# Kernel optimization log

Measured on AMD Instinct MI355X. Metric: run time of the kernel, lower is better.

## Reference

```python
import jax, jax.numpy as jnp
import numpy as np

N_ATOMS = 100_000   # atom_node.size(0)
N_EDGES = 3_200_000  # avg degree 32


def setup_inputs() -> dict:
    key = jax.random.key(0)
    k1, k2, k3, k4, k5 = jax.random.split(key, 5)
    disp = jax.random.normal(k1, (N_EDGES, 3), dtype=jnp.float32)
    a = jax.random.normal(k2, (N_EDGES,), dtype=jnp.float32)
    b = jax.random.normal(k3, (N_EDGES,), dtype=jnp.float32)
    edge_index = jax.random.randint(k4, (2, N_EDGES), 0, N_ATOMS, dtype=jnp.int64)
    atom_node = jax.random.randint(k5, (N_ATOMS,), 0, 100, dtype=jnp.int64)
    return {"disp": disp, "a": a, "b": b, "edge_index": edge_index, "atom_node": atom_node}


def _energy(disp, a, b):
    # surrogate differentiable per-edge energy: E = sum_e a_e*r2_e + b_e*exp(-r2_e)
    r2 = jnp.sum(disp * disp, axis=-1)  # [E]
    return jnp.sum(a * r2 + b * jnp.exp(-r2))


def reference(disp, a, b, edge_index, atom_node):
    n = atom_node.shape[0]
    # force = -dE/d(disp), create_graph analog: jax grads are differentiable
    force_edge = -jax.grad(_energy, argnums=0)(disp, a, b)  # [E,3]
    # dual scatter-add over the two endpoint index rows, then subtract
    f_src = jax.ops.segment_sum(force_edge, edge_index[0], num_segments=n)  # [N,3]
    f_dst = jax.ops.segment_sum(force_edge, edge_index[1], num_segments=n)  # [N,3]
    return f_src - f_dst
```

## Files before the change

kernel.cpp:

```cpp
#include <hip/hip_runtime.h>
#include <hip/hip_bf16.h>
#include <hip/hip_fp16.h>
#include <math.h>
#include <stdint.h>

constexpr int TPB         = 256;
constexpr int U           = 4;
constexpr int ROUND_EDGES = TPB * U;
constexpr int ROUND_REC   = ROUND_EDGES * 2;
constexpr int EPB         = 2048;
constexpr int NPB_SHIFT   = 10;
constexpr int NODES_PER_B = 1 << NPB_SHIFT;
constexpr int NB_MAX      = 128;
constexpr int CAPREC      = 80000;
constexpr int SPLIT       = 16;
constexpr int OCAP        = 262144;

__device__ __forceinline__ uint64_t pack_rec(int local, float fx, float fy, float fz) {
    uint64_t hx = __half_as_ushort(__float2half(fx));
    uint64_t hy = __half_as_ushort(__float2half(fy));
    uint64_t hz = __half_as_ushort(__float2half(fz));
    return (uint64_t)(unsigned)local | (hx << 16) | (hy << 32) | (hz << 48);
}

__global__ void __launch_bounds__(TPB)
p1_partition(const float* __restrict__ disp,
             const float* __restrict__ a,
             const float* __restrict__ b,
             const int* __restrict__ src,
             const int* __restrict__ dst,
             uint64_t* __restrict__ grecords,
             int* __restrict__ gcur,
             uint4* __restrict__ ovf,
             int* __restrict__ ovf_cnt,
             int E, int NB) {
    __shared__ int      s_cnt[NB_MAX];
    __shared__ int      s_off[NB_MAX];
    __shared__ int      s_gd[NB_MAX];
    __shared__ uint64_t s_rec[ROUND_REC];
    __shared__ uint8_t  s_bin[ROUND_REC];

    const int t = threadIdx.x;
    const int base = blockIdx.x * EPB;
    const int bend = min(base + EPB, E);

    for (int rb = base; rb < bend; rb += ROUND_EDGES) {
        const int rend = min(rb + ROUND_EDGES, bend);
        if (t < NB_MAX) s_cnt[t] = 0;
        __syncthreads();

        const int e0 = rb + t * U;
        float dxv[U], dyv[U], dzv[U], av[U], bv[U];
        int sv[U], dv[U];
        bool valid[U];
        if (e0 + U <= rend) {
            const float4* p = (const float4*)(disp + (size_t)3 * e0);
            float4 q0 = p[0], q1 = p[1], q2 = p[2];
            dxv[0] = q0.x; dyv[0] = q0.y; dzv[0] = q0.z;
            dxv[1] = q0.w; dyv[1] = q1.x; dzv[1] = q1.y;
            dxv[2] = q1.z; dyv[2] = q1.w; dzv[2] = q2.x;
            dxv[3] = q2.y; dyv[3] = q2.z; dzv[3] = q2.w;
            float4 qa = *(const float4*)(a + e0);
            av[0] = qa.x; av[1] = qa.y; av[2] = qa.z; av[3] = qa.w;
            float4 qb = *(const float4*)(b + e0);
            bv[0] = qb.x; bv[1] = qb.y; bv[2] = qb.z; bv[3] = qb.w;
            int4 qs = *(const int4*)(src + e0);
            sv[0] = qs.x; sv[1] = qs.y; sv[2] = qs.z; sv[3] = qs.w;
            int4 qd = *(const int4*)(dst + e0);
            dv[0] = qd.x; dv[1] = qd.y; dv[2] = qd.z; dv[3] = qd.w;
#pragma unroll
            for (int u = 0; u < U; ++u) valid[u] = true;
        } else {
#pragma unroll
            for (int u = 0; u < U; ++u) {
                int e = e0 + u;
                valid[u] = (e < rend);
                if (valid[u]) {
                    dxv[u] = disp[3 * e + 0];
                    dyv[u] = disp[3 * e + 1];
                    dzv[u] = disp[3 * e + 2];
                    av[u] = a[e]; bv[u] = b[e];
                    sv[u] = src[e]; dv[u] = dst[e];
                }
            }
        }

        uint64_t rec[2 * U];
        int rbin[2 * U], rrank[2 * U];
#pragma unroll
        for (int u = 0; u < U; ++u) {
            if (valid[u]) {
                float dx = dxv[u], dy = dyv[u], dz = dzv[u];
                float r2 = dx * dx + dy * dy + dz * dz;
                float coef = -2.0f * (av[u] - bv[u] * __expf(-r2));
                float fx = coef * dx, fy = coef * dy, fz = coef * dz;
                int nds[2] = { sv[u], dv[u] };
#pragma unroll
                for (int j = 0; j < 2; ++j) {
                    int k = 2 * u + j;
                    float s = j ? -1.0f : 1.0f;
                    int node = nds[j];
                    rec[k] = pack_rec(node & (NODES_PER_B - 1), s * fx, s * fy, s * fz);
                    rbin[k] = node >> NPB_SHIFT;
                    rrank[k] = atomicAdd(&s_cnt[rbin[k]], 1);
                }
            } else {
                rbin[2 * u] = -1; rbin[2 * u + 1] = -1;
            }
        }
        __syncthreads();

        if (t < 64) {
            int v0 = s_cnt[t];
            int v1 = s_cnt[64 + t];
#pragma unroll
            for (int d = 1; d < 64; d <<= 1) {
                int u0 = __shfl_up(v0, d, 64);
                int u1 = __shfl_up(v1, d, 64);
                if (t >= d) { v0 += u0; v1 += u1; }
            }
            int total0 = __shfl(v0, 63, 64);
            s_off[t] = v0;
            s_off[64 + t] = v1 + total0;
        }
        __syncthreads();

        if (t < NB) {
            int c = s_cnt[t];
            if (c > 0)
                s_gd[t] = atomicAdd(&gcur[t], c) - (s_off[t] - c);
        }
#pragma unroll
        for (int k = 0; k < 2 * U; ++k) {
            if (rbin[k] >= 0) {
                int pos = s_off[rbin[k]] - s_cnt[rbin[k]] + rrank[k];
                s_rec[pos] = rec[k];
                s_bin[pos] = (uint8_t)rbin[k];
            }
        }
        __syncthreads();

        const int total = s_off[NB_MAX - 1];
        for (int i = t; i < total; i += TPB) {
            uint64_t q = s_rec[i];
            int bin = (int)s_bin[i];
            int pos = s_gd[bin] + i;
            if ((unsigned)pos < (unsigned)CAPREC) {
                grecords[(size_t)bin * CAPREC + pos] = q;
            } else {
                int o = atomicAdd(ovf_cnt, 1);
                if (o < OCAP) {
                    uint4 v;
                    v.x = (unsigned)((bin << NPB_SHIFT) | (int)(q & (NODES_PER_B - 1)));
                    v.y = __float_as_uint(__half2float(__ushort_as_half((unsigned short)(q >> 16))));
                    v.z = __float_as_uint(__half2float(__ushort_as_half((unsigned short)(q >> 32))));
                    v.w = __float_as_uint(__half2float(__ushort_as_half((unsigned short)(q >> 48))));
                    ovf[o] = v;
                }
            }
        }
        __syncthreads();
    }
}

__device__ __forceinline__ uint64_t enc_xyz(float vx, float vy, float vz) {
    vx = fminf(fmaxf(vx, -63.0f), 63.0f);
    vy = fminf(fmaxf(vy, -63.0f), 63.0f);
    vz = fminf(fmaxf(vz, -63.0f), 63.0f);
    unsigned ex = (unsigned)((int)rintf(vx * 64.0f) + 4096);
    unsigned ey = (unsigned)((int)rintf(vy * 64.0f) + 4096);
    unsigned ez = (unsigned)((int)rintf(vz * 64.0f) + 4096);
    return (1ull << 54) | ((uint64_t)ez << 36) | ((uint64_t)ey << 18) | (uint64_t)ex;
}

__global__ void __launch_bounds__(TPB)
p2_reduce(const uint64_t* __restrict__ grecords,
          const int* __restrict__ gcur,
          float* __restrict__ partials,
          int NB) {
    __shared__ unsigned long long accA[NODES_PER_B];
    const int t = threadIdx.x;
    const int bucket = blockIdx.x >> 4;
    const int part   = blockIdx.x & (SPLIT - 1);

    for (int i = t; i < NODES_PER_B; i += TPB) accA[i] = 0ull;
    __syncthreads();

    int n = gcur[bucket];
    if (n > CAPREC) n = CAPREC;
    int lo = (int)((long long)n * part / SPLIT);
    int hi = (int)((long long)n * (part + 1) / SPLIT);
    const uint64_t* rbase = grecords + (size_t)bucket * CAPREC;

    int i = lo + t;
    for (; i + 3 * TPB < hi; i += 4 * TPB) {
        uint64_t q0 = rbase[i];
        uint64_t q1 = rbase[i + TPB];
        uint64_t q2 = rbase[i + 2 * TPB];
        uint64_t q3 = rbase[i + 3 * TPB];
#pragma unroll
        for (int u = 0; u < 4; ++u) {
            uint64_t q = (u == 0) ? q0 : (u == 1) ? q1 : (u == 2) ? q2 : q3;
            int local = (int)(q & (NODES_PER_B - 1));
            float vx = __half2float(__ushort_as_half((unsigned short)(q >> 16)));
            float vy = __half2float(__ushort_as_half((unsigned short)(q >> 32)));
            float vz = __half2float(__ushort_as_half((unsigned short)(q >> 48)));
            atomicAdd(&accA[local], (unsigned long long)enc_xyz(vx, vy, vz));
        }
    }
    for (; i < hi; i += TPB) {
        uint64_t q = rbase[i];
        int local = (int)(q & (NODES_PER_B - 1));
        float vx = __half2float(__ushort_as_half((unsigned short)(q >> 16)));
        float vy = __half2float(__ushort_as_half((unsigned short)(q >> 32)));
        float vz = __half2float(__ushort_as_half((unsigned short)(q >> 48)));
        atomicAdd(&accA[local], (unsigned long long)enc_xyz(vx, vy, vz));
    }
    __syncthreads();

    float* pb = partials + (size_t)part * ((size_t)NB * NODES_PER_B * 3)
              + (size_t)bucket * NODES_PER_B * 3;
    for (int k = t; k < NODES_PER_B; k += TPB) {
        uint64_t A = accA[k];
        float cnt = (float)(unsigned)(A >> 54);
        float xf = (float)(int)(A & 0x3FFFFull);
        float yf = (float)(int)((A >> 18) & 0x3FFFFull);
        float zf = (float)(int)((A >> 36) & 0x3FFFFull);
        float bias = cnt * 4096.0f;
        pb[k * 3 + 0] = (xf - bias) * (1.0f / 64.0f);
        pb[k * 3 + 1] = (yf - bias) * (1.0f / 64.0f);
        pb[k * 3 + 2] = (zf - bias) * (1.0f / 64.0f);
    }
}

__global__ void __launch_bounds__(TPB)
p4_sum_partials(const float* __restrict__ partials, float* __restrict__ out,
                int out_size, size_t pstride) {
    int i = blockIdx.x * blockDim.x + threadIdx.x;
    if (i >= out_size) return;
    float s = 0.0f;
#pragma unroll
    for (int p = 0; p < SPLIT; ++p)
        s += partials[(size_t)p * pstride + i];
    out[i] = s;
}

__global__ void __launch_bounds__(TPB)
p3_overflow(const uint4* __restrict__ ovf, const int* __restrict__ ovf_cnt,
            float* __restrict__ out) {
    int n = *ovf_cnt;
    if (n > OCAP) n = OCAP;
    int stride = gridDim.x * blockDim.x;
    for (int i = blockIdx.x * blockDim.x + threadIdx.x; i < n; i += stride) {
        uint4 r = ovf[i];
        int node = (int)r.x;
        unsafeAtomicAdd(&out[node * 3 + 0], __uint_as_float(r.y));
        unsafeAtomicAdd(&out[node * 3 + 1], __uint_as_float(r.z));
        unsafeAtomicAdd(&out[node * 3 + 2], __uint_as_float(r.w));
    }
}

__global__ void __launch_bounds__(TPB)
edge_force_scatter_direct(const float* __restrict__ disp,
                          const float* __restrict__ a,
                          const float* __restrict__ b,
                          const int* __restrict__ src,
                          const int* __restrict__ dst,
                          float* __restrict__ out,
                          int E) {
    int e = blockIdx.x * blockDim.x + threadIdx.x;
    if (e >= E) return;
    float dx = disp[3 * e + 0], dy = disp[3 * e + 1], dz = disp[3 * e + 2];
    float r2 = dx * dx + dy * dy + dz * dz;
    float coef = -2.0f * (a[e] - b[e] * __expf(-r2));
    float fx = coef * dx, fy = coef * dy, fz = coef * dz;
    int s = 3 * src[e], d = 3 * dst[e];
    unsafeAtomicAdd(&out[s + 0], fx);
    unsafeAtomicAdd(&out[s + 1], fy);
    unsafeAtomicAdd(&out[s + 2], fz);
    unsafeAtomicAdd(&out[d + 0], -fx);
    unsafeAtomicAdd(&out[d + 1], -fy);
    unsafeAtomicAdd(&out[d + 2], -fz);
}

extern "C" void kernel_launch(void* const* d_in, const int* in_sizes, int n_in,
                              void* d_out, int out_size, void* d_ws, size_t ws_size,
                              hipStream_t stream) {
    const float* disp = (const float*)d_in[0];
    const float* a    = (const float*)d_in[1];
    const float* b    = (const float*)d_in[2];
    const int*   ei   = (const int*)d_in[3];

    int E = in_sizes[1];
    int N = in_sizes[4];
    float* out = (float*)d_out;

    int NB = (N + NODES_PER_B - 1) >> NPB_SHIFT;
    int NBLK = (E + EPB - 1) / EPB;
    size_t pstride = (size_t)NB * NODES_PER_B * 3;

    size_t rec_bytes = (size_t)NB * CAPREC * sizeof(uint64_t);
    size_t need = 1024
                + rec_bytes
                + (size_t)OCAP * sizeof(uint4)
                + (size_t)SPLIT * pstride * sizeof(float);

    if (NB <= NB_MAX && ws_size >= need) {
        char* wsb = (char*)d_ws;
        int* gcur          = (int*)wsb;
        int* ovf_cnt       = (int*)(wsb + NB_MAX * sizeof(int));
        uint64_t* grecords = (uint64_t*)(wsb + 1024);
        uint4* ovf         = (uint4*)(wsb + 1024 + rec_bytes);
        float* partials    = (float*)((char*)ovf + (size_t)OCAP * sizeof(uint4));

        (void)hipMemsetAsync(wsb, 0, 1024, stream);

        p1_partition<<<NBLK, TPB, 0, stream>>>(
            disp, a, b, ei, ei + E, grecords, gcur, ovf, ovf_cnt, E, NB);
        p2_reduce<<<NB * SPLIT, TPB, 0, stream>>>(
            grecords, gcur, partials, NB);
        int grid4 = (out_size + TPB - 1) / TPB;
        p4_sum_partials<<<grid4, TPB, 0, stream>>>(partials, out, out_size, pstride);
        p3_overflow<<<64, TPB, 0, stream>>>(ovf, ovf_cnt, out);
    } else {
        (void)hipMemsetAsync(d_out, 0, (size_t)out_size * sizeof(float), stream);
        int grid = (E + TPB - 1) / TPB;
        edge_force_scatter_direct<<<grid, TPB, 0, stream>>>(
            disp, a, b, ei, ei + E, out, E);
    }
}
```

Measured before the change: 185.4 us.

## Replace global per-bucket atomic cursors with fixed per-block bucket slots

The partition kernel no longer does atomicAdd on a shared per-bucket cursor. Each block now writes its records into a private fixed-capacity slot region (CAP=56) per bucket and records its count. The reduce kernel walks all slots per bucket and skips empty entries using the per-block counts, with SPLIT cut from 16 to 8. This removes global atomic contention and makes write offsets deterministic. The cost is padded storage, wasted reads of empty slots and per-record divide/count checks, and blocks whose count exceeds CAP spill to the slower overflow path.

```diff
diff --git a/kernel.cpp b/kernel.cpp
--- a/kernel.cpp
+++ b/kernel.cpp
@@ -12,8 +12,8 @@
 constexpr int NPB_SHIFT   = 10;
 constexpr int NODES_PER_B = 1 << NPB_SHIFT;
 constexpr int NB_MAX      = 128;
-constexpr int CAPREC      = 80000;
-constexpr int SPLIT       = 16;
+constexpr int CAP         = 56;
+constexpr int SPLIT       = 8;
 constexpr int OCAP        = 262144;
 
 __device__ __forceinline__ uint64_t pack_rec(int local, float fx, float fy, float fz) {
@@ -30,10 +30,10 @@
              const int* __restrict__ src,
              const int* __restrict__ dst,
              uint64_t* __restrict__ grecords,
-             int* __restrict__ gcur,
+             int* __restrict__ gcnt,
              uint4* __restrict__ ovf,
              int* __restrict__ ovf_cnt,
-             int E, int NB) {
+             int E, int NB, int NBLK) {
     __shared__ int      s_cnt[NB_MAX];
     __shared__ int      s_off[NB_MAX];
     __shared__ int      s_gd[NB_MAX];
@@ -41,8 +41,11 @@
     __shared__ uint8_t  s_bin[ROUND_REC];
 
     const int t = threadIdx.x;
-    const int base = blockIdx.x * EPB;
+    const int blk = blockIdx.x;
+    const int base = blk * EPB;
     const int bend = min(base + EPB, E);
+
+    int wcur = 0;
 
     for (int rb = base; rb < bend; rb += ROUND_EDGES) {
         const int rend = min(rb + ROUND_EDGES, bend);
@@ -127,8 +130,8 @@
 
         if (t < NB) {
             int c = s_cnt[t];
-            if (c > 0)
-                s_gd[t] = atomicAdd(&gcur[t], c) - (s_off[t] - c);
+            s_gd[t] = wcur - (s_off[t] - c);
+            wcur += c;
         }
 #pragma unroll
         for (int k = 0; k < 2 * U; ++k) {
@@ -145,8 +148,8 @@
             uint64_t q = s_rec[i];
             int bin = (int)s_bin[i];
             int pos = s_gd[bin] + i;
-            if ((unsigned)pos < (unsigned)CAPREC) {
-                grecords[(size_t)bin * CAPREC + pos] = q;
+            if ((unsigned)pos < (unsigned)CAP) {
+                grecords[((size_t)bin * NBLK + blk) * CAP + pos] = q;
             } else {
                 int o = atomicAdd(ovf_cnt, 1);
                 if (o < OCAP) {
@@ -161,6 +164,8 @@
         }
         __syncthreads();
     }
+
+    if (t < NB) gcnt[(size_t)t * NBLK + blk] = min(wcur, CAP);
 }
 
 __device__ __forceinline__ uint64_t enc_xyz(float vx, float vy, float vz) {
@@ -175,46 +180,57 @@
 
 __global__ void __launch_bounds__(TPB)
 p2_reduce(const uint64_t* __restrict__ grecords,
-          const int* __restrict__ gcur,
+          const int* __restrict__ gcnt,
           float* __restrict__ partials,
-          int NB) {
+          int NB, int NBLK) {
     __shared__ unsigned long long accA[NODES_PER_B];
     const int t = threadIdx.x;
-    const int bucket = blockIdx.x >> 4;
+    const int bucket = blockIdx.x >> 3;
     const int part   = blockIdx.x & (SPLIT - 1);
 
     for (int i = t; i < NODES_PER_B; i += TPB) accA[i] = 0ull;
     __syncthreads();
 
-    int n = gcur[bucket];
-    if (n > CAPREC) n = CAPREC;
-    int lo = (int)((long long)n * part / SPLIT);
-    int hi = (int)((long long)n * (part + 1) / SPLIT);
-    const uint64_t* rbase = grecords + (size_t)bucket * CAPREC;
+    const int totslots = NBLK * CAP;
+    int lo = (int)((long long)totslots * part / SPLIT);
+    int hi = (int)((long long)totslots * (part + 1) / SPLIT);
+    const uint64_t* rbase = grecords + (size_t)bucket * totslots;
+    const int*      cbase = gcnt     + (size_t)bucket * NBLK;
 
     int i = lo + t;
     for (; i + 3 * TPB < hi; i += 4 * TPB) {
-        uint64_t q0 = rbase[i];
-        uint64_t q1 = rbase[i + TPB];
-        uint64_t q2 = rbase[i + 2 * TPB];
-        uint64_t q3 = rbase[i + 3 * TPB];
+        bool v[4]; uint64_t q[4];
 #pragma unroll
         for (int u = 0; u < 4; ++u) {
-            uint64_t q = (u == 0) ? q0 : (u == 1) ? q1 : (u == 2) ? q2 : q3;
-            int local = (int)(q & (NODES_PER_B - 1));
-            float vx = __half2float(__ushort_as_half((unsigned short)(q >> 16)));
-            float vy = __half2float(__ushort_as_half((unsigned short)(q >> 32)));
-            float vz = __half2float(__ushort_as_half((unsigned short)(q >> 48)));
+            int j = i + u * TPB;
+            int nb = j / CAP;
+            int slot = j - nb * CAP;
+            v[u] = slot < cbase[nb];
+            q[u] = v[u] ? rbase[j] : 0ull;
+        }
+#pragma unroll
+        for (int u = 0; u < 4; ++u) {
+            if (v[u]) {
+                uint64_t q0 = q[u];
+                int local = (int)(q0 & (NODES_PER_B - 1));
+                float vx = __half2float(__ushort_as_half((unsigned short)(q0 >> 16)));
+                float vy = __half2float(__ushort_as_half((unsigned short)(q0 >> 32)));
+                float vz = __half2float(__ushort_as_half((unsigned short)(q0 >> 48)));
+                atomicAdd(&accA[local], (unsigned long long)enc_xyz(vx, vy, vz));
+            }
+        }
+    }
+    for (; i < hi; i += TPB) {
+        int nb = i / CAP;
+        int slot = i - nb * CAP;
+        if (slot < cbase[nb]) {
+            uint64_t q0 = rbase[i];
+            int local = (int)(q0 & (NODES_PER_B - 1));
+            float vx = __half2float(__ushort_as_half((unsigned short)(q0 >> 16)));
+            float vy = __half2float(__ushort_as_half((unsigned short)(q0 >> 32)));
+            float vz = __half2float(__ushort_as_half((unsigned short)(q0 >> 48)));
             atomicAdd(&accA[local], (unsigned long long)enc_xyz(vx, vy, vz));
         }
-    }
-    for (; i < hi; i += TPB) {
-        uint64_t q = rbase[i];
-        int local = (int)(q & (NODES_PER_B - 1));
-        float vx = __half2float(__ushort_as_half((unsigned short)(q >> 16)));
-        float vy = __half2float(__ushort_as_half((unsigned short)(q >> 32)));
-        float vz = __half2float(__ushort_as_half((unsigned short)(q >> 48)));
-        atomicAdd(&accA[local], (unsigned long long)enc_xyz(vx, vy, vz));
     }
     __syncthreads();
 
@@ -299,26 +315,28 @@
     int NBLK = (E + EPB - 1) / EPB;
     size_t pstride = (size_t)NB * NODES_PER_B * 3;
 
-    size_t rec_bytes = (size_t)NB * CAPREC * sizeof(uint64_t);
-    size_t need = 1024
+    size_t gcnt_bytes = (((size_t)NB * NBLK * sizeof(int)) + 255) & ~(size_t)255;
+    size_t rec_bytes  = (size_t)NB * NBLK * CAP * sizeof(uint64_t);
+    size_t need = 256
+                + gcnt_bytes
                 + rec_bytes
                 + (size_t)OCAP * sizeof(uint4)
                 + (size_t)SPLIT * pstride * sizeof(float);
 
     if (NB <= NB_MAX && ws_size >= need) {
         char* wsb = (char*)d_ws;
-        int* gcur          = (int*)wsb;
-        int* ovf_cnt       = (int*)(wsb + NB_MAX * sizeof(int));
-        uint64_t* grecords = (uint64_t*)(wsb + 1024);
-        uint4* ovf         = (uint4*)(wsb + 1024 + rec_bytes);
+        int* ovf_cnt       = (int*)wsb;
+        int* gcnt          = (int*)(wsb + 256);
+        uint64_t* grecords = (uint64_t*)(wsb + 256 + gcnt_bytes);
+        uint4* ovf         = (uint4*)(wsb + 256 + gcnt_bytes + rec_bytes);
         float* partials    = (float*)((char*)ovf + (size_t)OCAP * sizeof(uint4));
 
-        (void)hipMemsetAsync(wsb, 0, 1024, stream);
+        (void)hipMemsetAsync(wsb, 0, 256, stream);
 
         p1_partition<<<NBLK, TPB, 0, stream>>>(
-            disp, a, b, ei, ei + E, grecords, gcur, ovf, ovf_cnt, E, NB);
+            disp, a, b, ei, ei + E, grecords, gcnt, ovf, ovf_cnt, E, NB, NBLK);
         p2_reduce<<<NB * SPLIT, TPB, 0, stream>>>(
-            grecords, gcur, partials, NB);
+            grecords, gcnt, partials, NB, NBLK);
         int grid4 = (out_size + TPB - 1) / TPB;
         p4_sum_partials<<<grid4, TPB, 0, stream>>>(partials, out, out_size, pstride);
         p3_overflow<<<64, TPB, 0, stream>>>(ovf, ovf_cnt, out);
```

After: 186.8 us. No clear change (+0.8%).
